# Optimization experiments

Hardware: AMD Instinct MI355X
Metric: run time of the kernel (lower is better)

The kernel has to match this reference:

```python
import jax, jax.numpy as jnp
import numpy as np

B, L, E, H, Dff = 2, 2048, 1024, 16, 4096
Dh = E // H


def _ln(x, g, b, eps=1e-5):
    m = jnp.mean(x, axis=-1, keepdims=True)
    v = jnp.mean((x - m) ** 2, axis=-1, keepdims=True)
    return (x - m) / jnp.sqrt(v + eps) * g + b


def setup_inputs() -> dict:
    key = jax.random.key(0)
    ks = jax.random.split(key, 16)
    s_e = 1.0 / np.sqrt(E)
    s_d = 1.0 / np.sqrt(Dff)
    inp = {
        "x": jax.random.normal(ks[0], (B, L, E), jnp.float32),
        # causal mask: positions with 0 are masked out (masked_fill(mask==0, -1e9))
        "mask": jnp.tril(jnp.ones((L, L), jnp.bool_)),
        # per-head QKV projections, stacked over heads: (H, E, Dh), biases (H, Dh)
        "Wq": jax.random.uniform(ks[1], (H, E, Dh), jnp.float32, -s_e, s_e),
        "bq": jax.random.uniform(ks[2], (H, Dh), jnp.float32, -s_e, s_e),
        "Wk": jax.random.uniform(ks[3], (H, E, Dh), jnp.float32, -s_e, s_e),
        "bk": jax.random.uniform(ks[4], (H, Dh), jnp.float32, -s_e, s_e),
        "Wv": jax.random.uniform(ks[5], (H, E, Dh), jnp.float32, -s_e, s_e),
        "bv": jax.random.uniform(ks[6], (H, Dh), jnp.float32, -s_e, s_e),
        "Wo": jax.random.uniform(ks[7], (E, E), jnp.float32, -s_e, s_e),
        "bo": jax.random.uniform(ks[8], (E,), jnp.float32, -s_e, s_e),
        "W1": jax.random.uniform(ks[9], (E, Dff), jnp.float32, -s_e, s_e),
        "c1": jax.random.uniform(ks[10], (Dff,), jnp.float32, -s_e, s_e),
        "W2": jax.random.uniform(ks[11], (Dff, E), jnp.float32, -s_d, s_d),
        "c2": jax.random.uniform(ks[12], (E,), jnp.float32, -s_d, s_d),
        "g1": jnp.ones((E,), jnp.float32),
        "beta1": jnp.zeros((E,), jnp.float32),
        "g2": jnp.ones((E,), jnp.float32),
        "beta2": jnp.zeros((E,), jnp.float32),
    }
    return inp


def reference(x, mask, Wq, bq, Wk, bk, Wv, bv, Wo, bo, W1, c1, W2, c2, g1, beta1, g2, beta2):
    # Batched equivalent of the per-head Attention loop (eval mode: dropout = identity)
    q = jnp.einsum("ble,hed->bhld", x, Wq) + bq[None, :, None, :]
    k = jnp.einsum("ble,hed->bhld", x, Wk) + bk[None, :, None, :]
    v = jnp.einsum("ble,hed->bhld", x, Wv) + bv[None, :, None, :]
    scores = jnp.einsum("bhld,bhmd->bhlm", q, k) / np.sqrt(Dh).astype(np.float32)
    scores = jnp.where(mask[None, None, :, :], scores, -1e9)
    p = jax.nn.softmax(scores, axis=-1)
    z = jnp.einsum("bhlm,bhmd->bhld", p, v)  # (B,H,L,Dh)
    z = z.transpose(0, 2, 1, 3).reshape(B, L, E)  # concat heads
    att = z @ Wo + bo
    h = _ln(x + att, g1, beta1)
    ff = jax.nn.relu(h @ W1 + c1) @ W2 + c2
    out = _ln(h + ff, g2, beta2)
    return out
```

## Files before the change

kernel.cpp:

```cpp
#include <hip/hip_runtime.h>
#include <hip/hip_bf16.h>
#include <math.h>

#define B_   2
#define L_   2048
#define E_   1024
#define H_   16
#define DH   64
#define DFF  4096
#define M_   4096
#define APAD 72
#define SCALE_Q 0.18033688011112042f

typedef __attribute__((ext_vector_type(8))) short short8;
typedef __attribute__((ext_vector_type(4))) float f32x4;
typedef __bf16 bf16x8 __attribute__((ext_vector_type(8)));

__device__ __forceinline__ float bf2f(unsigned short u) {
    return __uint_as_float(((unsigned)u) << 16);
}
__device__ __forceinline__ unsigned short f2bf(float f) {
    unsigned u = __float_as_uint(f);
    return (unsigned short)((u + 0x7fff + ((u >> 16) & 1)) >> 16);
}
__device__ __forceinline__ unsigned pk_trunc(float lo, float hi) {
    return (__float_as_uint(lo) >> 16) | (__float_as_uint(hi) & 0xffff0000u);
}

__device__ __forceinline__ void async16(const void* g, void* l) {
    __builtin_amdgcn_global_load_lds((const __attribute__((address_space(1))) void*)g,
                                     (__attribute__((address_space(3))) void*)l, 16, 0, 0);
}

__global__ __launch_bounds__(256) void prep(const float* __restrict__ x,
                                            const float* __restrict__ Wq,
                                            const float* __restrict__ Wk,
                                            const float* __restrict__ Wv,
                                            const float* __restrict__ bq,
                                            const float* __restrict__ bk,
                                            const float* __restrict__ bv,
                                            const float* __restrict__ Wo,
                                            const float* __restrict__ W1,
                                            const float* __restrict__ W2,
                                            unsigned short* __restrict__ xb,
                                            unsigned short* __restrict__ Wqkvt,
                                            unsigned short* __restrict__ Wot,
                                            unsigned short* __restrict__ W1t,
                                            unsigned short* __restrict__ W2t,
                                            float* __restrict__ bqkv) {
    __shared__ float tile[32][33];
    int bid = blockIdx.x;
    const int t = threadIdx.x;

    if (bid < 4096) {
        int i = (bid * 256 + t) * 4;
        float4 v = *(const float4*)&x[i];
        ushort4 pk = { f2bf(v.x), f2bf(v.y), f2bf(v.z), f2bf(v.w) };
        *(ushort4*)&xb[i] = pk;
        return;
    }
    bid -= 4096;

    const float* in; unsigned short* outp; int R, C, r0, c0; float sc = 1.f;
    if (bid < 3072) {
        int xq = bid & 1, yq = (bid >> 1) & 31, wh = bid >> 6;
        int which = wh >> 4, h = wh & 15;
        in   = (which == 0 ? Wq : which == 1 ? Wk : Wv) + (size_t)h * E_ * DH;
        outp = Wqkvt + ((size_t)which * 1024 + h * 64) * 1024;
        R = E_; C = DH; r0 = yq * 32; c0 = xq * 32;
        if (which == 0) sc = SCALE_Q;
    } else if (bid < 4096) {
        bid -= 3072;
        in = Wo; outp = Wot; R = E_; C = E_;
        c0 = (bid & 31) * 32; r0 = (bid >> 5) * 32;
    } else if (bid < 8192) {
        bid -= 4096;
        in = W1; outp = W1t; R = E_; C = DFF;
        c0 = (bid & 127) * 32; r0 = (bid >> 7) * 32;
    } else if (bid < 12288) {
        bid -= 8192;
        in = W2; outp = W2t; R = DFF; C = E_;
        c0 = (bid & 31) * 32; r0 = (bid >> 5) * 32;
    } else {
        bid -= 12288;
        int n = bid * 256 + t;
        bqkv[n] = n < 1024 ? bq[n] * SCALE_Q : n < 2048 ? bk[n - 1024] : bv[n - 2048];
        return;
    }

    const int tx = t & 31, tq = t >> 5;
#pragma unroll
    for (int s2 = 0; s2 < 4; s2++)
        tile[tq * 4 + s2][tx] = in[(size_t)(r0 + tq * 4 + s2) * C + c0 + tx] * sc;
    __syncthreads();
#pragma unroll
    for (int s2 = 0; s2 < 4; s2++)
        outp[(size_t)(c0 + tq * 4 + s2) * R + r0 + tx] = f2bf(tile[tx][tq * 4 + s2]);
}

__global__ __launch_bounds__(256) void v_transpose_perm(const unsigned short* __restrict__ qkv,
                                                        unsigned short* __restrict__ vtg) {
    __shared__ unsigned short tile[64 * APAD];
    const int t  = threadIdx.x;
    const int kt = blockIdx.x, hh = blockIdx.y, b = blockIdx.z;
    const int rr0 = t >> 3, o8 = (t & 7) * 8, rr1 = rr0 + 32;
    const size_t gbase = ((size_t)b * L_ + kt * 64) * 3072 + 2048 + hh * 64;
    *(short8*)&tile[rr0 * APAD + o8] = *(const short8*)&qkv[gbase + (size_t)rr0 * 3072 + o8];
    *(short8*)&tile[rr1 * APAD + o8] = *(const short8*)&qkv[gbase + (size_t)rr1 * 3072 + o8];
    __syncthreads();
    const size_t obase = ((size_t)(b * H_ + hh) * 64) * (size_t)L_ + kt * 64;
    const int a = t & 15, d0 = (t >> 4) * 4;
#pragma unroll
    for (int s2 = 0; s2 < 4; s2++) {
        int d = d0 + s2;
        ushort4 pk = { tile[(a +  0) * APAD + d], tile[(a + 16) * APAD + d],
                       tile[(a + 32) * APAD + d], tile[(a + 48) * APAD + d] };
        *(ushort4*)&vtg[obase + (size_t)d * L_ + 4 * a] = pk;
    }
}

template <int RELU, int OUT_BF16>
__global__ __launch_bounds__(256) void gemm_bt(const unsigned short* __restrict__ A,
                                               const unsigned short* __restrict__ Bt,
                                               const float* __restrict__ bias,
                                               void* __restrict__ Cout,
                                               int M, int N, int K) {
    __shared__ __align__(16) unsigned short As[128 * 32];
    __shared__ __align__(16) unsigned short Bs[128 * 32];

    const int t    = threadIdx.x;
    const int lane = t & 63;
    const int w    = t >> 6;
    const int quad = lane >> 4;
    const int l16  = lane & 15;
    const int wm = (w >> 1) * 64, wn = (w & 1) * 64;

    const int lin = blockIdx.x;
    const int xcd = lin & 7, s = lin >> 3;
    const int n0 = (s >> 2) * 128;
    const int m0 = ((xcd << 2) | (s & 3)) * 128;
    const int rowA = t >> 2, offA = (t & 3) * 8;

    f32x4 acc[4][4];
#pragma unroll
    for (int i = 0; i < 4; i++)
#pragma unroll
        for (int j = 0; j < 4; j++) acc[i][j] = (f32x4){0.f, 0.f, 0.f, 0.f};

    for (int k0 = 0; k0 < K; k0 += 32) {
        async16(&A[(size_t)(m0 + rowA) * K + k0 + offA],       &As[rowA * 32 + offA]);
        async16(&A[(size_t)(m0 + rowA + 64) * K + k0 + offA],  &As[(rowA + 64) * 32 + offA]);
        async16(&Bt[(size_t)(n0 + rowA) * K + k0 + offA],      &Bs[rowA * 32 + offA]);
        async16(&Bt[(size_t)(n0 + rowA + 64) * K + k0 + offA], &Bs[(rowA + 64) * 32 + offA]);
        __syncthreads();

        bf16x8 af[4], bfv[4];
#pragma unroll
        for (int i = 0; i < 4; i++)
            af[i] = *(const bf16x8*)&As[(wm + i * 16 + l16) * 32 + quad * 8];
#pragma unroll
        for (int j = 0; j < 4; j++)
            bfv[j] = *(const bf16x8*)&Bs[(wn + j * 16 + l16) * 32 + quad * 8];
#pragma unroll
        for (int i = 0; i < 4; i++)
#pragma unroll
            for (int j = 0; j < 4; j++)
                acc[i][j] = __builtin_amdgcn_mfma_f32_16x16x32_bf16(af[i], bfv[j], acc[i][j], 0, 0, 0);
        __syncthreads();
    }

#pragma unroll
    for (int j = 0; j < 4; j++) {
        int col = n0 + wn + j * 16 + l16;
        float bv = bias[col];
#pragma unroll
        for (int i = 0; i < 4; i++) {
            int rowb = m0 + wm + i * 16 + quad * 4;
#pragma unroll
            for (int r = 0; r < 4; r++) {
                float v = acc[i][j][r] + bv;
                if (RELU) v = fmaxf(v, 0.f);
                if (OUT_BF16)
                    ((unsigned short*)Cout)[(size_t)(rowb + r) * N + col] = f2bf(v);
                else
                    ((float*)Cout)[(size_t)(rowb + r) * N + col] = v;
            }
        }
    }
}

__global__ __launch_bounds__(256) void gemm_sk4(const unsigned short* __restrict__ A,
                                                const unsigned short* __restrict__ Bt,
                                                unsigned short* __restrict__ P0,
                                                unsigned short* __restrict__ P1,
                                                unsigned short* __restrict__ P2,
                                                unsigned short* __restrict__ P3,
                                                int M, int N, int K, int Nt) {
    __shared__ __align__(16) unsigned short As[128 * 32];
    __shared__ __align__(16) unsigned short Bs[128 * 32];

    const int t    = threadIdx.x;
    const int lane = t & 63;
    const int w    = t >> 6;
    const int quad = lane >> 4;
    const int l16  = lane & 15;
    const int wm = (w >> 1) * 64, wn = (w & 1) * 64;

    const int lin = blockIdx.x;
    const int xcd = lin & 7, s = lin >> 3;
    const int mi = s & 3;
    const int r  = s >> 2;
    const int n0 = (r % Nt) * 128;
    const int z  = r / Nt;
    const int m0 = ((xcd << 2) | mi) * 128;

    const int K4 = K >> 2;
    const int kbeg = z * K4;
    unsigned short* C = (z == 0) ? P0 : (z == 1) ? P1 : (z == 2) ? P2 : P3;
    const int rowA = t >> 2, offA = (t & 3) * 8;

    f32x4 acc[4][4];
#pragma unroll
    for (int i = 0; i < 4; i++)
#pragma unroll
        for (int j = 0; j < 4; j++) acc[i][j] = (f32x4){0.f, 0.f, 0.f, 0.f};

    for (int k0 = kbeg; k0 < kbeg + K4; k0 += 32) {
        async16(&A[(size_t)(m0 + rowA) * K + k0 + offA],       &As[rowA * 32 + offA]);
        async16(&A[(size_t)(m0 + rowA + 64) * K + k0 + offA],  &As[(rowA + 64) * 32 + offA]);
        async16(&Bt[(size_t)(n0 + rowA) * K + k0 + offA],      &Bs[rowA * 32 + offA]);
        async16(&Bt[(size_t)(n0 + rowA + 64) * K + k0 + offA], &Bs[(rowA + 64) * 32 + offA]);
        __syncthreads();

        bf16x8 af[4], bfv[4];
#pragma unroll
        for (int i = 0; i < 4; i++)
            af[i] = *(const bf16x8*)&As[(wm + i * 16 + l16) * 32 + quad * 8];
#pragma unroll
        for (int j = 0; j < 4; j++)
            bfv[j] = *(const bf16x8*)&Bs[(wn + j * 16 + l16) * 32 + quad * 8];
#pragma unroll
        for (int i = 0; i < 4; i++)
#pragma unroll
            for (int j = 0; j < 4; j++)
                acc[i][j] = __builtin_amdgcn_mfma_f32_16x16x32_bf16(af[i], bfv[j], acc[i][j], 0, 0, 0);
        __syncthreads();
    }

#pragma unroll
    for (int j = 0; j < 4; j++) {
        int col = n0 + wn + j * 16 + l16;
#pragma unroll
        for (int i = 0; i < 4; i++) {
            int rowb = m0 + wm + i * 16 + quad * 4;
#pragma unroll
            for (int r2 = 0; r2 < 4; r2++)
                C[(size_t)(rowb + r2) * N + col] = f2bf(acc[i][j][r2]);
        }
    }
}

__global__ __launch_bounds__(256, 3) void attn_mfma(const unsigned short* __restrict__ qkv,
                                                    const unsigned short* __restrict__ vtg,
                                                    unsigned short* __restrict__ zb) {
    __shared__ __align__(16) unsigned short ks[2][64 * APAD];
    __shared__ __align__(16) unsigned short vt[64 * APAD];
    __shared__ __align__(16) unsigned short ps[128 * APAD];

    const int t    = threadIdx.x;
    const int lane = t & 63;
    const int w    = t >> 6;
    const int l16  = lane & 15;
    const int quad = lane >> 4;

    const int lin  = blockIdx.x;
    const int xcd  = lin & 7;
    const int s    = lin >> 3;
    const int hh   = xcd * 2 + (s & 1);
    const int rest = s >> 1;
    const int b    = rest & 1;
    const int qq0  = rest >> 1;
    const int qq   = b ? qq0 : 15 - qq0;

    const size_t rowbase = (size_t)b * L_;
    const size_t vbase   = ((size_t)(b * H_ + hh) * 64) * (size_t)L_;

    bf16x8 qf[2][2];
#pragma unroll
    for (int g = 0; g < 2; g++) {
        size_t qrow = rowbase + qq * 128 + w * 32 + g * 16 + l16;
#pragma unroll
        for (int c = 0; c < 2; c++)
            qf[g][c] = *(const bf16x8*)&qkv[qrow * 3072 + hh * 64 + c * 32 + quad * 8];
    }

    f32x4 o[2][4];
#pragma unroll
    for (int g = 0; g < 2; g++)
#pragma unroll
        for (int j = 0; j < 4; j++) o[g][j] = (f32x4){0.f, 0.f, 0.f, 0.f};
    float l_i[2][4] = {};

    const int rr0 = t >> 3, o8 = (t & 7) * 8, rr1 = rr0 + 32;
    const int ktmax = 2 * qq + 1;

    {
        size_t kg = rowbase * 3072 + 1024 + hh * 64;
        short8 k0 = *(const short8*)&qkv[kg + (size_t)rr0 * 3072 + o8];
        short8 k1 = *(const short8*)&qkv[kg + (size_t)rr1 * 3072 + o8];
        short8 v0 = *(const short8*)&vtg[vbase + (size_t)rr0 * L_ + o8];
        short8 v1 = *(const short8*)&vtg[vbase + (size_t)rr1 * L_ + o8];
        *(short8*)&ks[0][rr0 * APAD + o8] = k0;
        *(short8*)&ks[0][rr1 * APAD + o8] = k1;
        *(short8*)&vt[rr0 * APAD + o8] = v0;
        *(short8*)&vt[rr1 * APAD + o8] = v1;
    }

    short8 kr0, kr1, vr0, vr1;
    for (int kt = 0; kt <= ktmax; kt++) {
        const int p = kt & 1;
        __syncthreads();

        if (kt < ktmax) {
            size_t kg = (rowbase + (kt + 1) * 64) * 3072 + 1024 + hh * 64;
            kr0 = *(const short8*)&qkv[kg + (size_t)rr0 * 3072 + o8];
            kr1 = *(const short8*)&qkv[kg + (size_t)rr1 * 3072 + o8];
            size_t vg = vbase + (kt + 1) * 64;
            vr0 = *(const short8*)&vtg[vg + (size_t)rr0 * L_ + o8];
            vr1 = *(const short8*)&vtg[vg + (size_t)rr1 * L_ + o8];
        }

        f32x4 s4[2][4];
#pragma unroll
        for (int g = 0; g < 2; g++)
#pragma unroll
            for (int j = 0; j < 4; j++) s4[g][j] = (f32x4){0.f, 0.f, 0.f, 0.f};
#pragma unroll
        for (int c = 0; c < 2; c++)
#pragma unroll
            for (int j = 0; j < 4; j++) {
                bf16x8 kf = *(const bf16x8*)&ks[p][(j * 16 + l16) * APAD + c * 32 + quad * 8];
#pragma unroll
                for (int g = 0; g < 2; g++)
                    s4[g][j] = __builtin_amdgcn_mfma_f32_16x16x32_bf16(qf[g][c], kf, s4[g][j], 0, 0, 0);
            }

        if (kt >= 2 * qq) {
#pragma unroll
            for (int g = 0; g < 2; g++)
#pragma unroll
                for (int j = 0; j < 4; j++) {
                    int lk = kt * 64 + j * 16 + l16;
#pragma unroll
                    for (int r = 0; r < 4; r++)
                        if (lk > qq * 128 + w * 32 + g * 16 + quad * 4 + r)
                            s4[g][j][r] = -INFINITY;
                }
        }

#pragma unroll
        for (int g = 0; g < 2; g++)
#pragma unroll
            for (int r = 0; r < 4; r++) {
                float p0 = __builtin_amdgcn_exp2f(s4[g][0][r]);
                float p1 = __builtin_amdgcn_exp2f(s4[g][1][r]);
                float p2 = __builtin_amdgcn_exp2f(s4[g][2][r]);
                float p3 = __builtin_amdgcn_exp2f(s4[g][3][r]);
                l_i[g][r] += (p0 + p1) + (p2 + p3);
                uint2 pk = { pk_trunc(p0, p1), pk_trunc(p2, p3) };
                *(uint2*)&ps[(w * 32 + g * 16 + quad * 4 + r) * APAD + 4 * l16] = pk;
            }

        __builtin_amdgcn_s_waitcnt(0xc07f);

#pragma unroll
        for (int c = 0; c < 2; c++) {
            bf16x8 pf[2];
#pragma unroll
            for (int g = 0; g < 2; g++)
                pf[g] = *(const bf16x8*)&ps[(w * 32 + g * 16 + l16) * APAD + c * 32 + quad * 8];
#pragma unroll
            for (int j = 0; j < 4; j++) {
                bf16x8 vf = *(const bf16x8*)&vt[(j * 16 + l16) * APAD + c * 32 + quad * 8];
#pragma unroll
                for (int g = 0; g < 2; g++)
                    o[g][j] = __builtin_amdgcn_mfma_f32_16x16x32_bf16(pf[g], vf, o[g][j], 0, 0, 0);
            }
        }

        __syncthreads();
        if (kt < ktmax) {
            *(short8*)&ks[p ^ 1][rr0 * APAD + o8] = kr0;
            *(short8*)&ks[p ^ 1][rr1 * APAD + o8] = kr1;
            *(short8*)&vt[rr0 * APAD + o8] = vr0;
            *(short8*)&vt[rr1 * APAD + o8] = vr1;
        }
    }

#pragma unroll
    for (int g = 0; g < 2; g++)
#pragma unroll
        for (int r = 0; r < 4; r++) {
            float l = l_i[g][r];
            l += __shfl_xor(l, 1);
            l += __shfl_xor(l, 2);
            l += __shfl_xor(l, 4);
            l += __shfl_xor(l, 8);
            float inv = 1.f / l;
            size_t row = rowbase + qq * 128 + w * 32 + g * 16 + quad * 4 + r;
#pragma unroll
            for (int j = 0; j < 4; j++)
                zb[row * 1024 + hh * 64 + j * 16 + l16] = f2bf(o[g][j][r] * inv);
        }
}

template <int WRITE_BF16>
__global__ __launch_bounds__(256) void ln5_kernel(const float* __restrict__ a,
                                                  const unsigned short* __restrict__ q0,
                                                  const unsigned short* __restrict__ q1,
                                                  const unsigned short* __restrict__ q2,
                                                  const unsigned short* __restrict__ q3,
                                                  const float* __restrict__ bias,
                                                  const float* __restrict__ g,
                                                  const float* __restrict__ be,
                                                  float* __restrict__ out,
                                                  unsigned short* __restrict__ out_bf) {
    __shared__ float s1[256], s2[256];
    const int row = blockIdx.x;
    const int t   = threadIdx.x;
    const size_t base = (size_t)row * E_ + t * 4;

    float4 ya = *(const float4*)&a[base];
    ushort4 u0 = *(const ushort4*)&q0[base];
    ushort4 u1 = *(const ushort4*)&q1[base];
    ushort4 u2 = *(const ushort4*)&q2[base];
    ushort4 u3 = *(const ushort4*)&q3[base];
    float4 bb = *(const float4*)&bias[t * 4];
    float y0 = ya.x + bb.x + bf2f(u0.x) + bf2f(u1.x) + bf2f(u2.x) + bf2f(u3.x);
    float y1 = ya.y + bb.y + bf2f(u0.y) + bf2f(u1.y) + bf2f(u2.y) + bf2f(u3.y);
    float y2 = ya.z + bb.z + bf2f(u0.z) + bf2f(u1.z) + bf2f(u2.z) + bf2f(u3.z);
    float y3 = ya.w + bb.w + bf2f(u0.w) + bf2f(u1.w) + bf2f(u2.w) + bf2f(u3.w);

    s1[t] = y0 + y1 + y2 + y3;
    s2[t] = y0 * y0 + y1 * y1 + y2 * y2 + y3 * y3;
    __syncthreads();
    for (int off = 128; off > 0; off >>= 1) {
        if (t < off) { s1[t] += s1[t + off]; s2[t] += s2[t + off]; }
        __syncthreads();
    }
    float mean = s1[0] * (1.0f / E_);
    float var  = s2[0] * (1.0f / E_) - mean * mean;
    float rstd = rsqrtf(var + 1e-5f);

    float4 gv = *(const float4*)&g[t * 4];
    float4 bv = *(const float4*)&be[t * 4];
    float4 ov;
    ov.x = (y0 - mean) * rstd * gv.x + bv.x;
    ov.y = (y1 - mean) * rstd * gv.y + bv.y;
    ov.z = (y2 - mean) * rstd * gv.z + bv.z;
    ov.w = (y3 - mean) * rstd * gv.w + bv.w;
    *(float4*)&out[base] = ov;
    if (WRITE_BF16) {
        ushort4 pk = { f2bf(ov.x), f2bf(ov.y), f2bf(ov.z), f2bf(ov.w) };
        *(ushort4*)&out_bf[base] = pk;
    }
}

extern "C" void kernel_launch(void* const* d_in, const int* in_sizes, int n_in,
                              void* d_out, int out_size, void* d_ws, size_t ws_size,
                              hipStream_t stream)
{
    const float* x     = (const float*)d_in[0];
    const float* Wq    = (const float*)d_in[2];
    const float* bq    = (const float*)d_in[3];
    const float* Wk    = (const float*)d_in[4];
    const float* bk    = (const float*)d_in[5];
    const float* Wv    = (const float*)d_in[6];
    const float* bv    = (const float*)d_in[7];
    const float* Wo    = (const float*)d_in[8];
    const float* bo    = (const float*)d_in[9];
    const float* W1    = (const float*)d_in[10];
    const float* c1    = (const float*)d_in[11];
    const float* W2    = (const float*)d_in[12];
    const float* c2    = (const float*)d_in[13];
    const float* g1    = (const float*)d_in[14];
    const float* beta1 = (const float*)d_in[15];
    const float* g2    = (const float*)d_in[16];
    const float* beta2 = (const float*)d_in[17];
    float* out = (float*)d_out;

    const size_t MB = 1024 * 1024;
    char* w = (char*)d_ws;
    unsigned short* xb    = (unsigned short*)(w + 0 * MB);
    unsigned short* Wqkvt = (unsigned short*)(w + 8 * MB);
    unsigned short* Wot   = (unsigned short*)(w + 14 * MB);
    unsigned short* W1t   = (unsigned short*)(w + 16 * MB);
    unsigned short* W2t   = (unsigned short*)(w + 24 * MB);
    float*          bqkv  = (float*)(w + 32 * MB);
    unsigned short* qkv   = (unsigned short*)(w + 33 * MB);
    unsigned short* zb    = (unsigned short*)(w + 57 * MB);
    float*          h     = (float*)(w + 65 * MB);
    unsigned short* vtg   = (unsigned short*)(w + 89 * MB);
    unsigned short* ap0   = (unsigned short*)(w + 33 * MB);
    unsigned short* ap1   = (unsigned short*)(w + 41 * MB);
    unsigned short* ap2   = (unsigned short*)(w + 49 * MB);
    unsigned short* ap3   = (unsigned short*)(w + 89 * MB);
    unsigned short* hb    = (unsigned short*)(w + 0 * MB);
    unsigned short* ff1b  = (unsigned short*)(w + 33 * MB);
    unsigned short* fp0   = (unsigned short*)(w + 0 * MB);
    unsigned short* fp1   = (unsigned short*)(w + 8 * MB);
    unsigned short* fp2   = (unsigned short*)(w + 16 * MB);
    unsigned short* fp3   = (unsigned short*)(w + 81 * MB);

    dim3 blk(256);

    prep<<<dim3(16396), blk, 0, stream>>>(x, Wq, Wk, Wv, bq, bk, bv, Wo, W1, W2,
                                          xb, Wqkvt, Wot, W1t, W2t, bqkv);

    gemm_bt<0, 1><<<dim3(768), blk, 0, stream>>>(xb, Wqkvt, bqkv, qkv, M_, 3072, E_);

    v_transpose_perm<<<dim3(L_ / 64, H_, B_), blk, 0, stream>>>(qkv, vtg);

    attn_mfma<<<dim3(512), blk, 0, stream>>>(qkv, vtg, zb);

    gemm_sk4<<<dim3(1024), blk, 0, stream>>>(zb, Wot, ap0, ap1, ap2, ap3, M_, E_, E_, 8);

    ln5_kernel<1><<<dim3(M_), blk, 0, stream>>>(x, ap0, ap1, ap2, ap3, bo, g1, beta1, h, hb);

    gemm_bt<1, 1><<<dim3(1024), blk, 0, stream>>>(hb, W1t, c1, ff1b, M_, DFF, E_);

    gemm_sk4<<<dim3(1024), blk, 0, stream>>>(ff1b, W2t, fp0, fp1, fp2, fp3, M_, E_, DFF, 8);

    ln5_kernel<0><<<dim3(M_), blk, 0, stream>>>(h, fp0, fp1, fp2, fp3, c2, g2, beta2, out, nullptr);
}
```

Before: 384.7 us.

## Double-buffer GEMM LDS tiles with register-staged prefetch of the next K tile

Both GEMM kernels no longer use direct global-to-LDS async loads followed by a barrier. They now keep two LDS buffers, load the next K tile into registers while MFMAs run on the current buffer, then write those registers to the other buffer before a single barrier per iteration. This hides global load latency behind compute and drops one barrier per iteration. In exchange it doubles LDS use, which may reduce occupancy, and adds register pressure plus explicit LDS store instructions.

Result: faster. 373.7 us (-2.9%).

```diff
diff --git a/kernel.cpp b/kernel.cpp
--- a/kernel.cpp
+++ b/kernel.cpp
@@ -25,11 +25,6 @@
 }
 __device__ __forceinline__ unsigned pk_trunc(float lo, float hi) {
     return (__float_as_uint(lo) >> 16) | (__float_as_uint(hi) & 0xffff0000u);
-}
-
-__device__ __forceinline__ void async16(const void* g, void* l) {
-    __builtin_amdgcn_global_load_lds((const __attribute__((address_space(1))) void*)g,
-                                     (__attribute__((address_space(3))) void*)l, 16, 0, 0);
 }
 
 __global__ __launch_bounds__(256) void prep(const float* __restrict__ x,
@@ -125,8 +120,8 @@
                                                const float* __restrict__ bias,
                                                void* __restrict__ Cout,
                                                int M, int N, int K) {
-    __shared__ __align__(16) unsigned short As[128 * 32];
-    __shared__ __align__(16) unsigned short Bs[128 * 32];
+    __shared__ __align__(16) unsigned short As[2][128 * 32];
+    __shared__ __align__(16) unsigned short Bs[2][128 * 32];
 
     const int t    = threadIdx.x;
     const int lane = t & 63;
@@ -139,7 +134,13 @@
     const int xcd = lin & 7, s = lin >> 3;
     const int n0 = (s >> 2) * 128;
     const int m0 = ((xcd << 2) | (s & 3)) * 128;
-    const int rowA = t >> 2, offA = (t & 3) * 8;
+    const int rowA = t >> 2, offA = (t & 3) * 8, rowA2 = rowA + 64;
+    const int la0 = rowA * 32 + offA, la1 = rowA2 * 32 + offA;
+
+    const size_t aoff0 = (size_t)(m0 + rowA)  * K + offA;
+    const size_t aoff1 = (size_t)(m0 + rowA2) * K + offA;
+    const size_t boff0 = (size_t)(n0 + rowA)  * K + offA;
+    const size_t boff1 = (size_t)(n0 + rowA2) * K + offA;
 
     f32x4 acc[4][4];
 #pragma unroll
@@ -147,25 +148,45 @@
 #pragma unroll
         for (int j = 0; j < 4; j++) acc[i][j] = (f32x4){0.f, 0.f, 0.f, 0.f};
 
-    for (int k0 = 0; k0 < K; k0 += 32) {
-        async16(&A[(size_t)(m0 + rowA) * K + k0 + offA],       &As[rowA * 32 + offA]);
-        async16(&A[(size_t)(m0 + rowA + 64) * K + k0 + offA],  &As[(rowA + 64) * 32 + offA]);
-        async16(&Bt[(size_t)(n0 + rowA) * K + k0 + offA],      &Bs[rowA * 32 + offA]);
-        async16(&Bt[(size_t)(n0 + rowA + 64) * K + k0 + offA], &Bs[(rowA + 64) * 32 + offA]);
-        __syncthreads();
+    short8 ra0 = *(const short8*)&A[aoff0];
+    short8 ra1 = *(const short8*)&A[aoff1];
+    short8 rb0 = *(const short8*)&Bt[boff0];
+    short8 rb1 = *(const short8*)&Bt[boff1];
+    *(short8*)&As[0][la0] = ra0;
+    *(short8*)&As[0][la1] = ra1;
+    *(short8*)&Bs[0][la0] = rb0;
+    *(short8*)&Bs[0][la1] = rb1;
+    __syncthreads();
+
+    int p = 0;
+    for (int k0 = 0; k0 < K; k0 += 32, p ^= 1) {
+        const bool more = (k0 + 32 < K);
+        if (more) {
+            ra0 = *(const short8*)&A[aoff0 + k0 + 32];
+            ra1 = *(const short8*)&A[aoff1 + k0 + 32];
+            rb0 = *(const short8*)&Bt[boff0 + k0 + 32];
+            rb1 = *(const short8*)&Bt[boff1 + k0 + 32];
+        }
 
         bf16x8 af[4], bfv[4];
 #pragma unroll
         for (int i = 0; i < 4; i++)
-            af[i] = *(const bf16x8*)&As[(wm + i * 16 + l16) * 32 + quad * 8];
+            af[i] = *(const bf16x8*)&As[p][(wm + i * 16 + l16) * 32 + quad * 8];
 #pragma unroll
         for (int j = 0; j < 4; j++)
-            bfv[j] = *(const bf16x8*)&Bs[(wn + j * 16 + l16) * 32 + quad * 8];
+            bfv[j] = *(const bf16x8*)&Bs[p][(wn + j * 16 + l16) * 32 + quad * 8];
 #pragma unroll
         for (int i = 0; i < 4; i++)
 #pragma unroll
             for (int j = 0; j < 4; j++)
                 acc[i][j] = __builtin_amdgcn_mfma_f32_16x16x32_bf16(af[i], bfv[j], acc[i][j], 0, 0, 0);
+
+        if (more) {
+            *(short8*)&As[p ^ 1][la0] = ra0;
+            *(short8*)&As[p ^ 1][la1] = ra1;
+            *(short8*)&Bs[p ^ 1][la0] = rb0;
+            *(short8*)&Bs[p ^ 1][la1] = rb1;
+        }
         __syncthreads();
     }
 
@@ -196,8 +217,8 @@
                                                 unsigned short* __restrict__ P2,
                                                 unsigned short* __restrict__ P3,
                                                 int M, int N, int K, int Nt) {
-    __shared__ __align__(16) unsigned short As[128 * 32];
-    __shared__ __align__(16) unsigned short Bs[128 * 32];
+    __shared__ __align__(16) unsigned short As[2][128 * 32];
+    __shared__ __align__(16) unsigned short Bs[2][128 * 32];
 
     const int t    = threadIdx.x;
     const int lane = t & 63;
@@ -217,7 +238,13 @@
     const int K4 = K >> 2;
     const int kbeg = z * K4;
     unsigned short* C = (z == 0) ? P0 : (z == 1) ? P1 : (z == 2) ? P2 : P3;
-    const int rowA = t >> 2, offA = (t & 3) * 8;
+    const int rowA = t >> 2, offA = (t & 3) * 8, rowA2 = rowA + 64;
+    const int la0 = rowA * 32 + offA, la1 = rowA2 * 32 + offA;
+
+    const size_t aoff0 = (size_t)(m0 + rowA)  * K + offA + kbeg;
+    const size_t aoff1 = (size_t)(m0 + rowA2) * K + offA + kbeg;
+    const size_t boff0 = (size_t)(n0 + rowA)  * K + offA + kbeg;
+    const size_t boff1 = (size_t)(n0 + rowA2) * K + offA + kbeg;
 
     f32x4 acc[4][4];
 #pragma unroll
@@ -225,25 +252,45 @@
 #pragma unroll
         for (int j = 0; j < 4; j++) acc[i][j] = (f32x4){0.f, 0.f, 0.f, 0.f};
 
-    for (int k0 = kbeg; k0 < kbeg + K4; k0 += 32) {
-        async16(&A[(size_t)(m0 + rowA) * K + k0 + offA],       &As[rowA * 32 + offA]);
-        async16(&A[(size_t)(m0 + rowA + 64) * K + k0 + offA],  &As[(rowA + 64) * 32 + offA]);
-        async16(&Bt[(size_t)(n0 + rowA) * K + k0 + offA],      &Bs[rowA * 32 + offA]);
-        async16(&Bt[(size_t)(n0 + rowA + 64) * K + k0 + offA], &Bs[(rowA + 64) * 32 + offA]);
-        __syncthreads();
+    short8 ra0 = *(const short8*)&A[aoff0];
+    short8 ra1 = *(const short8*)&A[aoff1];
+    short8 rb0 = *(const short8*)&Bt[boff0];
+    short8 rb1 = *(const short8*)&Bt[boff1];
+    *(short8*)&As[0][la0] = ra0;
+    *(short8*)&As[0][la1] = ra1;
+    *(short8*)&Bs[0][la0] = rb0;
+    *(short8*)&Bs[0][la1] = rb1;
+    __syncthreads();
+
+    int p = 0;
+    for (int k0 = 0; k0 < K4; k0 += 32, p ^= 1) {
+        const bool more = (k0 + 32 < K4);
+        if (more) {
+            ra0 = *(const short8*)&A[aoff0 + k0 + 32];
+            ra1 = *(const short8*)&A[aoff1 + k0 + 32];
+            rb0 = *(const short8*)&Bt[boff0 + k0 + 32];
+            rb1 = *(const short8*)&Bt[boff1 + k0 + 32];
+        }
 
         bf16x8 af[4], bfv[4];
 #pragma unroll
         for (int i = 0; i < 4; i++)
-            af[i] = *(const bf16x8*)&As[(wm + i * 16 + l16) * 32 + quad * 8];
+            af[i] = *(const bf16x8*)&As[p][(wm + i * 16 + l16) * 32 + quad * 8];
 #pragma unroll
         for (int j = 0; j < 4; j++)
-            bfv[j] = *(const bf16x8*)&Bs[(wn + j * 16 + l16) * 32 + quad * 8];
+            bfv[j] = *(const bf16x8*)&Bs[p][(wn + j * 16 + l16) * 32 + quad * 8];
 #pragma unroll
         for (int i = 0; i < 4; i++)
 #pragma unroll
             for (int j = 0; j < 4; j++)
                 acc[i][j] = __builtin_amdgcn_mfma_f32_16x16x32_bf16(af[i], bfv[j], acc[i][j], 0, 0, 0);
+
+        if (more) {
+            *(short8*)&As[p ^ 1][la0] = ra0;
+            *(short8*)&As[p ^ 1][la1] = ra1;
+            *(short8*)&Bs[p ^ 1][la0] = rb0;
+            *(short8*)&Bs[p ^ 1][la1] = rb1;
+        }
         __syncthreads();
     }
 
```
